# Performance work log

Hardware: AMD Instinct MI355X
Metric: run time of the kernel (lower is better)

The kernel has to match this reference:

```python
import jax, jax.numpy as jnp
import numpy as np

N_NODES = 100000
N_EDGES = 50000
NNZ = 1600000
D = 128
EPS = 1e-6

def setup_inputs() -> dict:
    key = jax.random.key(0)
    k1, k2, k3, k4 = jax.random.split(key, 4)
    return {
        "t": jnp.zeros((), dtype=jnp.float32),
        "y": jax.random.normal(k1, (N_NODES, D), dtype=jnp.float32),
        "W": jax.random.normal(k2, (D, D), dtype=jnp.float32) / np.sqrt(D),
        "b": jnp.zeros((D,), dtype=jnp.float32),
        "inc_nodes": jax.random.randint(k3, (NNZ,), 0, N_NODES),
        "inc_edges": jax.random.randint(k4, (NNZ,), 0, N_EDGES),
    }

def reference(t, y, W, b, inc_nodes, inc_edges):
    # --- manifold projection (unit hypersphere): correct numerical drift ---
    norm = jnp.sqrt(jnp.sum(y * y, axis=-1, keepdims=True))
    yp = y / jnp.maximum(norm, EPS)  # [n, d]

    # --- hypergraph conv: linear transform then incidence aggregation ---
    xw = yp @ W  # [n, d_out]

    ones = jnp.ones((inc_nodes.shape[0],), dtype=xw.dtype)
    # node -> hyperedge (mean over member nodes)
    e_sum = jax.ops.segment_sum(xw[inc_nodes], inc_edges, num_segments=N_EDGES)  # [m, d]
    e_deg = jax.ops.segment_sum(ones, inc_edges, num_segments=N_EDGES)
    e_feat = e_sum / jnp.maximum(e_deg, 1.0)[:, None]

    # hyperedge -> node (mean over incident hyperedges)
    n_sum = jax.ops.segment_sum(e_feat[inc_edges], inc_nodes, num_segments=N_NODES)  # [n, d]
    n_deg = jax.ops.segment_sum(ones, inc_nodes, num_segments=N_NODES)
    out = n_sum / jnp.maximum(n_deg, 1.0)[:, None] + b

    # --- activation ---
    return jax.nn.relu(out)
```

## Files before the change

### kernel.cpp

```cpp
#include <hip/hip_runtime.h>
#include <hip/hip_fp16.h>

#define D 128
#define N_EDGES_C 50000
#define EPART_BITS 10
#define NPART_BITS 11
#define NPARTS 49
#define STAGE_CAP 36864
#define CAP_E 96
#define CAP_N 48
#define SLICES 4
#define SCAP 9216
#define NB_E 1024
#define NB_N 2048

typedef _Float16 f16x8 __attribute__((ext_vector_type(8)));
typedef float f32x4 __attribute__((ext_vector_type(4)));

__global__ __launch_bounds__(256) void k_prep(
    const int* __restrict__ inodes, const int* __restrict__ iedges,
    unsigned* __restrict__ e_stage, unsigned* __restrict__ n_stage,
    int* __restrict__ cursors, int nnz, int nb_part,
    const float* __restrict__ y, const float* __restrict__ W,
    __half* __restrict__ y_h, __half* __restrict__ Wt, int n_nodes)
{
    __shared__ int h[98];
    __shared__ int base[98];
    if ((int)blockIdx.x < nb_part) {
        const int t0 = blockIdx.x * 4096;
        const int tn = min(4096, nnz - t0);
        if (tn <= 0) return;
        for (int i = threadIdx.x; i < 98; i += 256) h[i] = 0;
        __syncthreads();
        int ev[16], nv[16];
        unsigned valid = 0;
        #pragma unroll
        for (int u = 0; u < 16; ++u) {
            int i = threadIdx.x + u * 256;
            int e = 0, nd = 0;
            if (i < tn) {
                e = __builtin_nontemporal_load(&iedges[t0 + i]);
                nd = __builtin_nontemporal_load(&inodes[t0 + i]);
                atomicAdd(&h[e >> EPART_BITS], 1);
                atomicAdd(&h[49 + (nd >> NPART_BITS)], 1);
                valid |= (1u << u);
            }
            ev[u] = e;
            nv[u] = nd;
        }
        __syncthreads();
        for (int i = threadIdx.x; i < 98; i += 256) base[i] = atomicAdd(&cursors[i], h[i]);
        __syncthreads();
        for (int i = threadIdx.x; i < 98; i += 256) h[i] = base[i];
        __syncthreads();
        #pragma unroll
        for (int u = 0; u < 16; ++u) {
            if (valid & (1u << u)) {
                int e = ev[u], nd = nv[u];
                int pe = e >> EPART_BITS;
                int pn = nd >> NPART_BITS;
                int re = atomicAdd(&h[pe], 1);
                if (re < STAGE_CAP)
                    e_stage[(size_t)pe * STAGE_CAP + re] = ((unsigned)(e & 1023) << 17) | (unsigned)nd;
                int rn = atomicAdd(&h[49 + pn], 1);
                if (rn < STAGE_CAP)
                    n_stage[(size_t)pn * STAGE_CAP + rn] = ((unsigned)(nd & 2047) << 16) | (unsigned)e;
            }
        }
        return;
    }
    if ((int)blockIdx.x == nb_part) {
        const int c = threadIdx.x & 127;
        const int k0 = (threadIdx.x >> 7) * 64;
        for (int k = k0; k < k0 + 64; ++k)
            Wt[c * D + k] = __float2half(W[(size_t)k * D + c]);
        return;
    }
    const int wv = threadIdx.x >> 6;
    const int lane = threadIdx.x & 63;
    const int row = ((int)blockIdx.x - nb_part - 1) * 4 + wv;
    if (row >= n_nodes) return;
    float2 v = reinterpret_cast<const float2*>(y + (size_t)row * D)[lane];
    float ss = v.x * v.x + v.y * v.y;
    #pragma unroll
    for (int off = 32; off >= 1; off >>= 1) ss += __shfl_xor(ss, off, 64);
    float inv = 1.0f / fmaxf(sqrtf(ss), 1e-6f);
    reinterpret_cast<__half2*>(y_h + (size_t)row * D)[lane] =
        __floats2half2_rn(v.x * inv, v.y * inv);
}

__global__ __launch_bounds__(256) void k_mm(const __half* __restrict__ y_h,
                                            const __half* __restrict__ Wt,
                                            __half* __restrict__ xw,
                                            int n_nodes) {
    __shared__ _Float16 Bl[128 * 136];
    for (int i = threadIdx.x; i < 2048; i += 256) {
        int c = i >> 4, seg = i & 15;
        *reinterpret_cast<f16x8*>(&Bl[c * 136 + seg * 8]) =
            *reinterpret_cast<const f16x8*>(Wt + c * D + seg * 8);
    }
    __syncthreads();
    const int wv = threadIdx.x >> 6;
    const int lane = threadIdx.x & 63;
    const int r0 = blockIdx.x * 64 + wv * 16;
    const int arow = min(r0 + (lane & 15), n_nodes - 1);
    const f16x8* ap = reinterpret_cast<const f16x8*>(y_h + (size_t)arow * D + (lane >> 4) * 8);
    f16x8 a0 = ap[0], a1 = ap[4], a2 = ap[8], a3 = ap[12];

    f32x4 acc[8];
    #pragma unroll
    for (int ct = 0; ct < 8; ++ct) acc[ct] = f32x4{0.f, 0.f, 0.f, 0.f};

    #pragma unroll
    for (int ct = 0; ct < 8; ++ct) {
        const int c = ct * 16 + (lane & 15);
        const f16x8* bp = reinterpret_cast<const f16x8*>(&Bl[c * 136 + (lane >> 4) * 8]);
        f16x8 b0 = bp[0], b1 = bp[4], b2 = bp[8], b3 = bp[12];
        acc[ct] = __builtin_amdgcn_mfma_f32_16x16x32_f16(a0, b0, acc[ct], 0, 0, 0);
        acc[ct] = __builtin_amdgcn_mfma_f32_16x16x32_f16(a1, b1, acc[ct], 0, 0, 0);
        acc[ct] = __builtin_amdgcn_mfma_f32_16x16x32_f16(a2, b2, acc[ct], 0, 0, 0);
        acc[ct] = __builtin_amdgcn_mfma_f32_16x16x32_f16(a3, b3, acc[ct], 0, 0, 0);
    }
    #pragma unroll
    for (int reg = 0; reg < 4; ++reg) {
        const int row = r0 + (lane >> 4) * 4 + reg;
        if (row < n_nodes) {
            #pragma unroll
            for (int ct = 0; ct < 8; ++ct)
                xw[(size_t)row * D + ct * 16 + (lane & 15)] = __float2half(acc[ct][reg]);
        }
    }
}

__global__ __launch_bounds__(512) void k_sort(const unsigned* __restrict__ e_stage,
                                              const unsigned* __restrict__ n_stage,
                                              const int* __restrict__ cursors,
                                              int* __restrict__ e_cur,
                                              int* __restrict__ n_cur,
                                              unsigned* __restrict__ adj_e,
                                              unsigned short* __restrict__ adj_n,
                                              int n_edges, int n_nodes) {
    __shared__ unsigned buf[SCAP];
    __shared__ int hist[NB_N];
    __shared__ int base[NB_N];
    __shared__ int cur[NB_N];
    __shared__ int wsum[8];
    const int side = (int)blockIdx.x >= NPARTS * SLICES;
    const int rem = side ? blockIdx.x - NPARTS * SLICES : blockIdx.x;
    const int p = rem / SLICES;
    const int q = rem % SLICES;
    const int NB = side ? NB_N : NB_E;
    const int SHIFT = side ? 16 : 17;
    const int total = min(cursors[(side ? 49 : 0) + p], STAGE_CAP);
    const int chunk = (total + SLICES - 1) / SLICES;
    const int lo = q * chunk;
    const int cnt_rec = max(0, min(chunk, total - lo));
    const unsigned* st = (side ? n_stage : e_stage) + (size_t)p * STAGE_CAP + lo;

    for (int i = threadIdx.x; i < NB; i += 512) hist[i] = 0;
    __syncthreads();
    for (int i = threadIdx.x; i < cnt_rec; i += 512)
        atomicAdd(&hist[st[i] >> SHIFT], 1);
    __syncthreads();
    const int bper = NB >> 9;
    int tsum = 0;
    for (int j = 0; j < bper; ++j) tsum += hist[threadIdx.x * bper + j];
    const int lane = threadIdx.x & 63;
    const int wv = threadIdx.x >> 6;
    int sc = tsum;
    #pragma unroll
    for (int o = 1; o < 64; o <<= 1) {
        int v = __shfl_up(sc, o, 64);
        if (lane >= o) sc += v;
    }
    if (lane == 63) wsum[wv] = sc;
    __syncthreads();
    int woff = 0;
    for (int w = 0; w < wv; ++w) woff += wsum[w];
    int run = woff + sc - tsum;
    for (int j = 0; j < bper; ++j) {
        int bi = threadIdx.x * bper + j;
        base[bi] = run;
        run += hist[bi];
    }
    __syncthreads();
    const int row0 = side ? (p << NPART_BITS) : (p << EPART_BITS);
    const int nrows = side ? n_nodes : n_edges;
    int* rcur = side ? n_cur : e_cur;
    for (int i = threadIdx.x; i < NB; i += 512) {
        cur[i] = base[i];
        int hh = hist[i];
        int g = 0;
        if (hh > 0 && row0 + i < nrows) g = atomicAdd(&rcur[row0 + i], hh);
        hist[i] = g;
    }
    __syncthreads();
    for (int i = threadIdx.x; i < cnt_rec; i += 512) {
        unsigned w = st[i];
        int pos = atomicAdd(&cur[w >> SHIFT], 1);
        buf[pos] = w;
    }
    __syncthreads();
    for (int j = threadIdx.x; j < cnt_rec; j += 512) {
        unsigned w = buf[j];
        int bin = (int)(w >> SHIFT);
        int g = hist[bin] + (j - base[bin]);
        if (!side) {
            if (g < CAP_E) adj_e[(size_t)(row0 + bin) * CAP_E + g] = w & 0x1FFFFu;
        } else {
            if (g < CAP_N) adj_n[(size_t)(row0 + bin) * CAP_N + g] = (unsigned short)(w & 0xFFFFu);
        }
    }
}

__global__ __launch_bounds__(256) void k_seg_e(const __half* __restrict__ xw,
                                               const unsigned* __restrict__ adj_e,
                                               const int* __restrict__ e_cnt,
                                               __half* __restrict__ e_feat,
                                               int n_edges) {
    const int wave = (blockIdx.x * 256 + threadIdx.x) >> 6;
    const int lane = threadIdx.x & 63;
    if (wave >= n_edges) return;
    const int deg = e_cnt[wave];
    const int cnt = min(deg, CAP_E);
    const unsigned* bucket = adj_e + (size_t)wave * CAP_E;
    const int slot = lane >> 4;
    const int c16 = lane & 15;
    float acc[8];
    #pragma unroll
    for (int j = 0; j < 8; ++j) acc[j] = 0.f;
    for (int base = 0; base < cnt; base += 4) {
        const int i = base + slot;
        if (i < cnt) {
            const unsigned m = bucket[i];
            f16x8 v = *reinterpret_cast<const f16x8*>(xw + (size_t)m * D + c16 * 8);
            #pragma unroll
            for (int j = 0; j < 8; ++j) acc[j] += (float)v[j];
        }
    }
    #pragma unroll
    for (int off = 16; off <= 32; off <<= 1) {
        #pragma unroll
        for (int j = 0; j < 8; ++j) acc[j] += __shfl_xor(acc[j], off, 64);
    }
    if (slot == 0) {
        const float inv = 1.0f / fmaxf((float)deg, 1.0f);
        f16x8 h;
        #pragma unroll
        for (int j = 0; j < 8; ++j) h[j] = (_Float16)(acc[j] * inv);
        *reinterpret_cast<f16x8*>(e_feat + (size_t)wave * D + c16 * 8) = h;
    }
}

__global__ __launch_bounds__(256) void k_seg_n(const __half* __restrict__ e_feat,
                                               const unsigned short* __restrict__ adj_n,
                                               const int* __restrict__ n_cnt,
                                               const float* __restrict__ bias,
                                               float* __restrict__ out,
                                               int n_nodes) {
    const int wave = (blockIdx.x * 256 + threadIdx.x) >> 6;
    const int lane = threadIdx.x & 63;
    if (wave >= n_nodes) return;
    const int deg = n_cnt[wave];
    const int cnt = min(deg, CAP_N);
    const unsigned short* bucket = adj_n + (size_t)wave * CAP_N;
    const int slot = lane >> 4;
    const int c16 = lane & 15;
    float acc[8];
    #pragma unroll
    for (int j = 0; j < 8; ++j) acc[j] = 0.f;
    for (int base = 0; base < cnt; base += 4) {
        const int i = base + slot;
        if (i < cnt) {
            const int m = (int)bucket[i];
            f16x8 v = *reinterpret_cast<const f16x8*>(e_feat + (size_t)m * D + c16 * 8);
            #pragma unroll
            for (int j = 0; j < 8; ++j) acc[j] += (float)v[j];
        }
    }
    #pragma unroll
    for (int off = 16; off <= 32; off <<= 1) {
        #pragma unroll
        for (int j = 0; j < 8; ++j) acc[j] += __shfl_xor(acc[j], off, 64);
    }
    if (slot == 0) {
        const float inv = 1.0f / fmaxf((float)deg, 1.0f);
        float4 b0 = reinterpret_cast<const float4*>(bias)[c16 * 2];
        float4 b1 = reinterpret_cast<const float4*>(bias)[c16 * 2 + 1];
        float4 o0, o1;
        o0.x = fmaxf(fmaf(acc[0], inv, b0.x), 0.f);
        o0.y = fmaxf(fmaf(acc[1], inv, b0.y), 0.f);
        o0.z = fmaxf(fmaf(acc[2], inv, b0.z), 0.f);
        o0.w = fmaxf(fmaf(acc[3], inv, b0.w), 0.f);
        o1.x = fmaxf(fmaf(acc[4], inv, b1.x), 0.f);
        o1.y = fmaxf(fmaf(acc[5], inv, b1.y), 0.f);
        o1.z = fmaxf(fmaf(acc[6], inv, b1.z), 0.f);
        o1.w = fmaxf(fmaf(acc[7], inv, b1.w), 0.f);
        float4* dst = reinterpret_cast<float4*>(out + (size_t)wave * D + c16 * 8);
        dst[0] = o0;
        dst[1] = o1;
    }
}

extern "C" void kernel_launch(void* const* d_in, const int* in_sizes, int n_in,
                              void* d_out, int out_size, void* d_ws, size_t ws_size,
                              hipStream_t stream) {
    const float* y = (const float*)d_in[1];
    const float* W = (const float*)d_in[2];
    const float* b = (const float*)d_in[3];
    const int* inodes = (const int*)d_in[4];
    const int* iedges = (const int*)d_in[5];
    const int nnz = in_sizes[4];
    const int n_nodes = in_sizes[1] / D;
    const int n_edges = N_EDGES_C;
    float* out = (float*)d_out;

    char* base = (char*)d_ws;
    const size_t XW_B  = (size_t)n_nodes * D * 2;
    const size_t STG_B = (size_t)2 * NPARTS * STAGE_CAP * 4;
    const size_t YH_B  = (size_t)n_nodes * D * 2;
    __half* xw       = (__half*)base;
    unsigned* e_stage = (unsigned*)(base + XW_B);
    unsigned* n_stage = e_stage + (size_t)NPARTS * STAGE_CAP;
    __half* e_feat   = (__half*)e_stage;
    __half* y_h      = (__half*)(base + XW_B + STG_B);
    unsigned* adj_e  = (unsigned*)y_h;
    unsigned short* adj_n = (unsigned short*)(base + XW_B + STG_B + YH_B);
    int* e_cur   = (int*)(adj_n + (size_t)n_nodes * CAP_N);
    int* n_cur   = e_cur + n_edges;
    int* cursors = n_cur + n_nodes;
    __half* Wt   = (__half*)(cursors + 112);

    hipMemsetAsync(e_cur, 0, (size_t)(n_edges + n_nodes + 112) * sizeof(int), stream);

    const int nb_part = (nnz + 4095) / 4096;
    const int nb_ynorm = (n_nodes + 3) / 4;
    k_prep<<<nb_part + 1 + nb_ynorm, 256, 0, stream>>>(inodes, iedges, e_stage, n_stage,
                                                       cursors, nnz, nb_part,
                                                       y, W, y_h, Wt, n_nodes);
    k_mm<<<(n_nodes + 63) / 64, 256, 0, stream>>>(y_h, Wt, xw, n_nodes);
    k_sort<<<2 * NPARTS * SLICES, 512, 0, stream>>>(e_stage, n_stage, cursors,
                                                    e_cur, n_cur, adj_e, adj_n,
                                                    n_edges, n_nodes);
    k_seg_e<<<(n_edges * 64 + 255) / 256, 256, 0, stream>>>(xw, adj_e, e_cur, e_feat, n_edges);
    k_seg_n<<<(n_nodes * 64 + 255) / 256, 256, 0, stream>>>(e_feat, adj_n, n_cur, b, out, n_nodes);
}
```

Measured before the change: 202.4 us.

## Fuse normalization into matmul, merge matmul with sort, unroll gathers

Row normalization of y moves out of the prep kernel and into the MFMA matmul, which now reads fp32 y directly, so the fp16 y_h intermediate is gone. The matmul and the bucket-sort kernels become one launch, with block ranges split by role and sharing one raw shared-memory buffer, so the sort can overlap the GEMM. Both segment-gather kernels now issue four independent row loads per iteration and point out-of-range slots at a zeroed padding row instead of branching. This removes one kernel launch and the y_h round trip and adds memory-level parallelism. In exchange the workspace layout changes and the merged kernel's larger shared-memory footprint may lower occupancy.

```diff
diff --git a/kernel.cpp b/kernel.cpp
--- a/kernel.cpp
+++ b/kernel.cpp
@@ -13,6 +13,7 @@
 #define SCAP 9216
 #define NB_E 1024
 #define NB_N 2048
+#define NSORT (2 * NPARTS * SLICES)
 
 typedef _Float16 f16x8 __attribute__((ext_vector_type(8)));
 typedef float f32x4 __attribute__((ext_vector_type(4)));
@@ -21,8 +22,7 @@
     const int* __restrict__ inodes, const int* __restrict__ iedges,
     unsigned* __restrict__ e_stage, unsigned* __restrict__ n_stage,
     int* __restrict__ cursors, int nnz, int nb_part,
-    const float* __restrict__ y, const float* __restrict__ W,
-    __half* __restrict__ y_h, __half* __restrict__ Wt, int n_nodes)
+    const float* __restrict__ W, __half* __restrict__ Wt)
 {
     __shared__ int h[98];
     __shared__ int base[98];
@@ -69,32 +69,101 @@
         }
         return;
     }
-    if ((int)blockIdx.x == nb_part) {
-        const int c = threadIdx.x & 127;
-        const int k0 = (threadIdx.x >> 7) * 64;
-        for (int k = k0; k < k0 + 64; ++k)
-            Wt[c * D + k] = __float2half(W[(size_t)k * D + c]);
+    const int c = threadIdx.x & 127;
+    const int k0 = (threadIdx.x >> 7) * 64;
+    for (int k = k0; k < k0 + 64; ++k)
+        Wt[c * D + k] = __float2half(W[(size_t)k * D + c]);
+}
+
+__global__ __launch_bounds__(512) void k_mm_sort(
+    const unsigned* __restrict__ e_stage, const unsigned* __restrict__ n_stage,
+    const int* __restrict__ cursors,
+    int* __restrict__ e_cur, int* __restrict__ n_cur,
+    unsigned* __restrict__ adj_e, unsigned short* __restrict__ adj_n,
+    int n_edges, int n_nodes,
+    const float* __restrict__ y, const __half* __restrict__ Wt,
+    __half* __restrict__ xw)
+{
+    __shared__ __align__(16) char smem[61504];
+    if ((int)blockIdx.x < NSORT) {
+        unsigned* buf = (unsigned*)smem;
+        int* hist = (int*)(smem + SCAP * 4);
+        int* base_ = hist + NB_N;
+        int* cur = base_ + NB_N;
+        int* wsum = cur + NB_N;
+        const int side = (int)blockIdx.x >= NPARTS * SLICES;
+        const int rem = side ? blockIdx.x - NPARTS * SLICES : blockIdx.x;
+        const int p = rem / SLICES;
+        const int q = rem % SLICES;
+        const int NB = side ? NB_N : NB_E;
+        const int SHIFT = side ? 16 : 17;
+        const int total = min(cursors[(side ? 49 : 0) + p], STAGE_CAP);
+        const int chunk = (total + SLICES - 1) / SLICES;
+        const int lo = q * chunk;
+        const int cnt_rec = max(0, min(chunk, total - lo));
+        const unsigned* st = (side ? n_stage : e_stage) + (size_t)p * STAGE_CAP + lo;
+
+        for (int i = threadIdx.x; i < NB; i += 512) hist[i] = 0;
+        __syncthreads();
+        for (int i = threadIdx.x; i < cnt_rec; i += 512)
+            atomicAdd(&hist[st[i] >> SHIFT], 1);
+        __syncthreads();
+        const int bper = NB >> 9;
+        int tsum = 0;
+        for (int j = 0; j < bper; ++j) tsum += hist[threadIdx.x * bper + j];
+        const int lane = threadIdx.x & 63;
+        const int wv = threadIdx.x >> 6;
+        int sc = tsum;
+        #pragma unroll
+        for (int o = 1; o < 64; o <<= 1) {
+            int v = __shfl_up(sc, o, 64);
+            if (lane >= o) sc += v;
+        }
+        if (lane == 63) wsum[wv] = sc;
+        __syncthreads();
+        int woff = 0;
+        for (int w = 0; w < wv; ++w) woff += wsum[w];
+        int run = woff + sc - tsum;
+        for (int j = 0; j < bper; ++j) {
+            int bi = threadIdx.x * bper + j;
+            base_[bi] = run;
+            run += hist[bi];
+        }
+        __syncthreads();
+        const int row0 = side ? (p << NPART_BITS) : (p << EPART_BITS);
+        const int nrows = side ? n_nodes : n_edges;
+        int* rcur = side ? n_cur : e_cur;
+        for (int i = threadIdx.x; i < NB; i += 512) {
+            cur[i] = base_[i];
+            int hh = hist[i];
+            int g = 0;
+            if (hh > 0 && row0 + i < nrows) g = atomicAdd(&rcur[row0 + i], hh);
+            hist[i] = g;
+        }
+        __syncthreads();
+        for (int i = threadIdx.x; i < cnt_rec; i += 512) {
+            unsigned w = st[i];
+            int pos = atomicAdd(&cur[w >> SHIFT], 1);
+            buf[pos] = w;
+        }
+        __syncthreads();
+        for (int j = threadIdx.x; j < cnt_rec; j += 512) {
+            unsigned w = buf[j];
+            int bin = (int)(w >> SHIFT);
+            int g = hist[bin] + (j - base_[bin]);
+            if (!side) {
+                if (g < CAP_E) adj_e[(size_t)(row0 + bin) * CAP_E + g] = w & 0x1FFFFu;
+            } else {
+                if (g < CAP_N) adj_n[(size_t)(row0 + bin) * CAP_N + g] = (unsigned short)(w & 0xFFFFu);
+            }
+        }
         return;
     }
-    const int wv = threadIdx.x >> 6;
-    const int lane = threadIdx.x & 63;
-    const int row = ((int)blockIdx.x - nb_part - 1) * 4 + wv;
-    if (row >= n_nodes) return;
-    float2 v = reinterpret_cast<const float2*>(y + (size_t)row * D)[lane];
-    float ss = v.x * v.x + v.y * v.y;
-    #pragma unroll
-    for (int off = 32; off >= 1; off >>= 1) ss += __shfl_xor(ss, off, 64);
-    float inv = 1.0f / fmaxf(sqrtf(ss), 1e-6f);
-    reinterpret_cast<__half2*>(y_h + (size_t)row * D)[lane] =
-        __floats2half2_rn(v.x * inv, v.y * inv);
-}
-
-__global__ __launch_bounds__(256) void k_mm(const __half* __restrict__ y_h,
-                                            const __half* __restrict__ Wt,
-                                            __half* __restrict__ xw,
-                                            int n_nodes) {
-    __shared__ _Float16 Bl[128 * 136];
-    for (int i = threadIdx.x; i < 2048; i += 256) {
+    const int bid = blockIdx.x - NSORT;
+    if (bid == 0 && threadIdx.x < D)
+        xw[(size_t)n_nodes * D + threadIdx.x] = __float2half(0.f);
+    _Float16* Bl = (_Float16*)smem;
+    for (int i = threadIdx.x; i < 2048; i += 512) {
         int c = i >> 4, seg = i & 15;
         *reinterpret_cast<f16x8*>(&Bl[c * 136 + seg * 8]) =
             *reinterpret_cast<const f16x8*>(Wt + c * D + seg * 8);
@@ -102,113 +171,54 @@
     __syncthreads();
     const int wv = threadIdx.x >> 6;
     const int lane = threadIdx.x & 63;
-    const int r0 = blockIdx.x * 64 + wv * 16;
-    const int arow = min(r0 + (lane & 15), n_nodes - 1);
-    const f16x8* ap = reinterpret_cast<const f16x8*>(y_h + (size_t)arow * D + (lane >> 4) * 8);
-    f16x8 a0 = ap[0], a1 = ap[4], a2 = ap[8], a3 = ap[12];
+    const int r0 = bid * 128 + wv * 16;
+    const int s = lane >> 4;
+    const int r16 = lane & 15;
+    const int row = min(r0 + r16, n_nodes - 1);
+    const float* yr = y + (size_t)row * D;
+    float v[4][8];
+    float ss = 0.f;
+    #pragma unroll
+    for (int c = 0; c < 4; ++c) {
+        f32x4 u0 = *reinterpret_cast<const f32x4*>(yr + c * 32 + s * 8);
+        f32x4 u1 = *reinterpret_cast<const f32x4*>(yr + c * 32 + s * 8 + 4);
+        #pragma unroll
+        for (int j = 0; j < 4; ++j) {
+            v[c][j] = u0[j];
+            v[c][4 + j] = u1[j];
+            ss = fmaf(u0[j], u0[j], ss);
+            ss = fmaf(u1[j], u1[j], ss);
+        }
+    }
+    ss += __shfl_xor(ss, 16, 64);
+    ss += __shfl_xor(ss, 32, 64);
+    const float inv = 1.0f / fmaxf(sqrtf(ss), 1e-6f);
+    f16x8 a[4];
+    #pragma unroll
+    for (int c = 0; c < 4; ++c)
+        #pragma unroll
+        for (int j = 0; j < 8; ++j) a[c][j] = (_Float16)(v[c][j] * inv);
 
     f32x4 acc[8];
     #pragma unroll
     for (int ct = 0; ct < 8; ++ct) acc[ct] = f32x4{0.f, 0.f, 0.f, 0.f};
-
     #pragma unroll
     for (int ct = 0; ct < 8; ++ct) {
-        const int c = ct * 16 + (lane & 15);
-        const f16x8* bp = reinterpret_cast<const f16x8*>(&Bl[c * 136 + (lane >> 4) * 8]);
+        const int c = ct * 16 + r16;
+        const f16x8* bp = reinterpret_cast<const f16x8*>(&Bl[c * 136 + s * 8]);
         f16x8 b0 = bp[0], b1 = bp[4], b2 = bp[8], b3 = bp[12];
-        acc[ct] = __builtin_amdgcn_mfma_f32_16x16x32_f16(a0, b0, acc[ct], 0, 0, 0);
-        acc[ct] = __builtin_amdgcn_mfma_f32_16x16x32_f16(a1, b1, acc[ct], 0, 0, 0);
-        acc[ct] = __builtin_amdgcn_mfma_f32_16x16x32_f16(a2, b2, acc[ct], 0, 0, 0);
-        acc[ct] = __builtin_amdgcn_mfma_f32_16x16x32_f16(a3, b3, acc[ct], 0, 0, 0);
+        acc[ct] = __builtin_amdgcn_mfma_f32_16x16x32_f16(a[0], b0, acc[ct], 0, 0, 0);
+        acc[ct] = __builtin_amdgcn_mfma_f32_16x16x32_f16(a[1], b1, acc[ct], 0, 0, 0);
+        acc[ct] = __builtin_amdgcn_mfma_f32_16x16x32_f16(a[2], b2, acc[ct], 0, 0, 0);
+        acc[ct] = __builtin_amdgcn_mfma_f32_16x16x32_f16(a[3], b3, acc[ct], 0, 0, 0);
     }
     #pragma unroll
     for (int reg = 0; reg < 4; ++reg) {
-        const int row = r0 + (lane >> 4) * 4 + reg;
-        if (row < n_nodes) {
+        const int orow = r0 + s * 4 + reg;
+        if (orow < n_nodes) {
             #pragma unroll
             for (int ct = 0; ct < 8; ++ct)
-                xw[(size_t)row * D + ct * 16 + (lane & 15)] = __float2half(acc[ct][reg]);
-        }
-    }
-}
-
-__global__ __launch_bounds__(512) void k_sort(const unsigned* __restrict__ e_stage,
-                                              const unsigned* __restrict__ n_stage,
-                                              const int* __restrict__ cursors,
-                                              int* __restrict__ e_cur,
-                                              int* __restrict__ n_cur,
-                                              unsigned* __restrict__ adj_e,
-                                              unsigned short* __restrict__ adj_n,
-                                              int n_edges, int n_nodes) {
-    __shared__ unsigned buf[SCAP];
-    __shared__ int hist[NB_N];
-    __shared__ int base[NB_N];
-    __shared__ int cur[NB_N];
-    __shared__ int wsum[8];
-    const int side = (int)blockIdx.x >= NPARTS * SLICES;
-    const int rem = side ? blockIdx.x - NPARTS * SLICES : blockIdx.x;
-    const int p = rem / SLICES;
-    const int q = rem % SLICES;
-    const int NB = side ? NB_N : NB_E;
-    const int SHIFT = side ? 16 : 17;
-    const int total = min(cursors[(side ? 49 : 0) + p], STAGE_CAP);
-    const int chunk = (total + SLICES - 1) / SLICES;
-    const int lo = q * chunk;
-    const int cnt_rec = max(0, min(chunk, total - lo));
-    const unsigned* st = (side ? n_stage : e_stage) + (size_t)p * STAGE_CAP + lo;
-
-    for (int i = threadIdx.x; i < NB; i += 512) hist[i] = 0;
-    __syncthreads();
-    for (int i = threadIdx.x; i < cnt_rec; i += 512)
-        atomicAdd(&hist[st[i] >> SHIFT], 1);
-    __syncthreads();
-    const int bper = NB >> 9;
-    int tsum = 0;
-    for (int j = 0; j < bper; ++j) tsum += hist[threadIdx.x * bper + j];
-    const int lane = threadIdx.x & 63;
-    const int wv = threadIdx.x >> 6;
-    int sc = tsum;
-    #pragma unroll
-    for (int o = 1; o < 64; o <<= 1) {
-        int v = __shfl_up(sc, o, 64);
-        if (lane >= o) sc += v;
-    }
-    if (lane == 63) wsum[wv] = sc;
-    __syncthreads();
-    int woff = 0;
-    for (int w = 0; w < wv; ++w) woff += wsum[w];
-    int run = woff + sc - tsum;
-    for (int j = 0; j < bper; ++j) {
-        int bi = threadIdx.x * bper + j;
-        base[bi] = run;
-        run += hist[bi];
-    }
-    __syncthreads();
-    const int row0 = side ? (p << NPART_BITS) : (p << EPART_BITS);
-    const int nrows = side ? n_nodes : n_edges;
-    int* rcur = side ? n_cur : e_cur;
-    for (int i = threadIdx.x; i < NB; i += 512) {
-        cur[i] = base[i];
-        int hh = hist[i];
-        int g = 0;
-        if (hh > 0 && row0 + i < nrows) g = atomicAdd(&rcur[row0 + i], hh);
-        hist[i] = g;
-    }
-    __syncthreads();
-    for (int i = threadIdx.x; i < cnt_rec; i += 512) {
-        unsigned w = st[i];
-        int pos = atomicAdd(&cur[w >> SHIFT], 1);
-        buf[pos] = w;
-    }
-    __syncthreads();
-    for (int j = threadIdx.x; j < cnt_rec; j += 512) {
-        unsigned w = buf[j];
-        int bin = (int)(w >> SHIFT);
-        int g = hist[bin] + (j - base[bin]);
-        if (!side) {
-            if (g < CAP_E) adj_e[(size_t)(row0 + bin) * CAP_E + g] = w & 0x1FFFFu;
-        } else {
-            if (g < CAP_N) adj_n[(size_t)(row0 + bin) * CAP_N + g] = (unsigned short)(w & 0xFFFFu);
+                xw[(size_t)orow * D + ct * 16 + r16] = __float2half(acc[ct][reg]);
         }
     }
 }
@@ -217,7 +227,9 @@
                                                const unsigned* __restrict__ adj_e,
                                                const int* __restrict__ e_cnt,
                                                __half* __restrict__ e_feat,
-                                               int n_edges) {
+                                               int n_edges, int zrow) {
+    if (blockIdx.x == 0 && threadIdx.x < D)
+        e_feat[(size_t)n_edges * D + threadIdx.x] = __float2half(0.f);
     const int wave = (blockIdx.x * 256 + threadIdx.x) >> 6;
     const int lane = threadIdx.x & 63;
     if (wave >= n_edges) return;
@@ -229,19 +241,26 @@
     float acc[8];
     #pragma unroll
     for (int j = 0; j < 8; ++j) acc[j] = 0.f;
-    for (int base = 0; base < cnt; base += 4) {
-        const int i = base + slot;
-        if (i < cnt) {
-            const unsigned m = bucket[i];
-            f16x8 v = *reinterpret_cast<const f16x8*>(xw + (size_t)m * D + c16 * 8);
-            #pragma unroll
-            for (int j = 0; j < 8; ++j) acc[j] += (float)v[j];
-        }
-    }
-    #pragma unroll
-    for (int off = 16; off <= 32; off <<= 1) {
-        #pragma unroll
-        for (int j = 0; j < 8; ++j) acc[j] += __shfl_xor(acc[j], off, 64);
+    for (int base = 0; base < cnt; base += 16) {
+        const int i0 = base + slot;
+        int m0 = (i0      < cnt) ? (int)bucket[i0]      : zrow;
+        int m1 = (i0 + 4  < cnt) ? (int)bucket[i0 + 4]  : zrow;
+        int m2 = (i0 + 8  < cnt) ? (int)bucket[i0 + 8]  : zrow;
+        int m3 = (i0 + 12 < cnt) ? (int)bucket[i0 + 12] : zrow;
+        f16x8 v0 = *reinterpret_cast<const f16x8*>(xw + (size_t)m0 * D + c16 * 8);
+        f16x8 v1 = *reinterpret_cast<const f16x8*>(xw + (size_t)m1 * D + c16 * 8);
+        f16x8 v2 = *reinterpret_cast<const f16x8*>(xw + (size_t)m2 * D + c16 * 8);
+        f16x8 v3 = *reinterpret_cast<const f16x8*>(xw + (size_t)m3 * D + c16 * 8);
+        #pragma unroll
+        for (int j = 0; j < 8; ++j) {
+            acc[j] += (float)v0[j] + (float)v1[j];
+            acc[j] += (float)v2[j] + (float)v3[j];
+        }
+    }
+    #pragma unroll
+    for (int j = 0; j < 8; ++j) {
+        acc[j] += __shfl_xor(acc[j], 16, 64);
+        acc[j] += __shfl_xor(acc[j], 32, 64);
     }
     if (slot == 0) {
         const float inv = 1.0f / fmaxf((float)deg, 1.0f);
@@ -257,7 +276,7 @@
                                                const int* __restrict__ n_cnt,
                                                const float* __restrict__ bias,
                                                float* __restrict__ out,
-                                               int n_nodes) {
+                                               int n_nodes, int zrow) {
     const int wave = (blockIdx.x * 256 + threadIdx.x) >> 6;
     const int lane = threadIdx.x & 63;
     if (wave >= n_nodes) return;
@@ -269,19 +288,26 @@
     float acc[8];
     #pragma unroll
     for (int j = 0; j < 8; ++j) acc[j] = 0.f;
-    for (int base = 0; base < cnt; base += 4) {
-        const int i = base + slot;
-        if (i < cnt) {
-            const int m = (int)bucket[i];
-            f16x8 v = *reinterpret_cast<const f16x8*>(e_feat + (size_t)m * D + c16 * 8);
-            #pragma unroll
-            for (int j = 0; j < 8; ++j) acc[j] += (float)v[j];
-        }
-    }
-    #pragma unroll
-    for (int off = 16; off <= 32; off <<= 1) {
-        #pragma unroll
-        for (int j = 0; j < 8; ++j) acc[j] += __shfl_xor(acc[j], off, 64);
+    for (int base = 0; base < cnt; base += 16) {
+        const int i0 = base + slot;
+        int m0 = (i0      < cnt) ? (int)bucket[i0]      : zrow;
+        int m1 = (i0 + 4  < cnt) ? (int)bucket[i0 + 4]  : zrow;
+        int m2 = (i0 + 8  < cnt) ? (int)bucket[i0 + 8]  : zrow;
+        int m3 = (i0 + 12 < cnt) ? (int)bucket[i0 + 12] : zrow;
+        f16x8 v0 = *reinterpret_cast<const f16x8*>(e_feat + (size_t)m0 * D + c16 * 8);
+        f16x8 v1 = *reinterpret_cast<const f16x8*>(e_feat + (size_t)m1 * D + c16 * 8);
+        f16x8 v2 = *reinterpret_cast<const f16x8*>(e_feat + (size_t)m2 * D + c16 * 8);
+        f16x8 v3 = *reinterpret_cast<const f16x8*>(e_feat + (size_t)m3 * D + c16 * 8);
+        #pragma unroll
+        for (int j = 0; j < 8; ++j) {
+            acc[j] += (float)v0[j] + (float)v1[j];
+            acc[j] += (float)v2[j] + (float)v3[j];
+        }
+    }
+    #pragma unroll
+    for (int j = 0; j < 8; ++j) {
+        acc[j] += __shfl_xor(acc[j], 16, 64);
+        acc[j] += __shfl_xor(acc[j], 32, 64);
     }
     if (slot == 0) {
         const float inv = 1.0f / fmaxf((float)deg, 1.0f);
@@ -315,33 +341,33 @@
     const int n_edges = N_EDGES_C;
     float* out = (float*)d_out;
 
-    char* base = (char*)d_ws;
-    const size_t XW_B  = (size_t)n_nodes * D * 2;
-    const size_t STG_B = (size_t)2 * NPARTS * STAGE_CAP * 4;
-    const size_t YH_B  = (size_t)n_nodes * D * 2;
-    __half* xw       = (__half*)base;
-    unsigned* e_stage = (unsigned*)(base + XW_B);
+    char* p = (char*)d_ws;
+    __half* xw = (__half*)p;
+    p += (size_t)(n_nodes + 8) * D * 2;
+    unsigned* e_stage = (unsigned*)p;
     unsigned* n_stage = e_stage + (size_t)NPARTS * STAGE_CAP;
-    __half* e_feat   = (__half*)e_stage;
-    __half* y_h      = (__half*)(base + XW_B + STG_B);
-    unsigned* adj_e  = (unsigned*)y_h;
-    unsigned short* adj_n = (unsigned short*)(base + XW_B + STG_B + YH_B);
-    int* e_cur   = (int*)(adj_n + (size_t)n_nodes * CAP_N);
-    int* n_cur   = e_cur + n_edges;
+    __half* e_feat = (__half*)e_stage;
+    p += (size_t)2 * NPARTS * STAGE_CAP * 4;
+    unsigned* adj_e = (unsigned*)p;
+    p += (size_t)n_edges * CAP_E * 4;
+    unsigned short* adj_n = (unsigned short*)p;
+    p += (size_t)n_nodes * CAP_N * 2;
+    int* e_cur = (int*)p;
+    int* n_cur = e_cur + n_edges;
     int* cursors = n_cur + n_nodes;
-    __half* Wt   = (__half*)(cursors + 112);
+    __half* Wt = (__half*)(cursors + 112);
 
     hipMemsetAsync(e_cur, 0, (size_t)(n_edges + n_nodes + 112) * sizeof(int), stream);
 
     const int nb_part = (nnz + 4095) / 4096;
-    const int nb_ynorm = (n_nodes + 3) / 4;
-    k_prep<<<nb_part + 1 + nb_ynorm, 256, 0, stream>>>(inodes, iedges, e_stage, n_stage,
-                                                       cursors, nnz, nb_part,
-                                                       y, W, y_h, Wt, n_nodes);
-    k_mm<<<(n_nodes + 63) / 64, 256, 0, stream>>>(y_h, Wt, xw, n_nodes);
-    k_sort<<<2 * NPARTS * SLICES, 512, 0, stream>>>(e_stage, n_stage, cursors,
-                                                    e_cur, n_cur, adj_e, adj_n,
-                                                    n_edges, n_nodes);
-    k_seg_e<<<(n_edges * 64 + 255) / 256, 256, 0, stream>>>(xw, adj_e, e_cur, e_feat, n_edges);
-    k_seg_n<<<(n_nodes * 64 + 255) / 256, 256, 0, stream>>>(e_feat, adj_n, n_cur, b, out, n_nodes);
-}
+    k_prep<<<nb_part + 1, 256, 0, stream>>>(inodes, iedges, e_stage, n_stage,
+                                            cursors, nnz, nb_part, W, Wt);
+    const int nt_mm = (n_nodes + 127) / 128;
+    k_mm_sort<<<NSORT + nt_mm, 512, 0, stream>>>(e_stage, n_stage, cursors,
+                                                 e_cur, n_cur, adj_e, adj_n,
+                                                 n_edges, n_nodes, y, Wt, xw);
+    k_seg_e<<<(n_edges * 64 + 255) / 256, 256, 0, stream>>>(xw, adj_e, e_cur,
+                                                            e_feat, n_edges, n_nodes);
+    k_seg_n<<<(n_nodes * 64 + 255) / 256, 256, 0, stream>>>(e_feat, adj_n, n_cur,
+                                                            b, out, n_nodes, n_edges);
+}
```

New measurement: 172.3 us, median of 2. 14.9% less time.
